# Kernel optimization log

Measured on AMD Instinct MI355X. Metric: run time of the kernel, lower is better.

The kernel has to match this reference:

```python
import jax, jax.numpy as jnp
import numpy as np

BATCH, SEQ, H, N = 8, 4096, 512, 64
DT_MIN, DT_MAX = 1e-3, 1e-1


def setup_inputs() -> dict:
    key = jax.random.key(0)
    k1, k2, k3, k4, k5 = jax.random.split(key, 5)
    n = jnp.arange(N, dtype=jnp.float32)
    # HiPPO-LegS diagonal: A[n,n] = -(n+1) -> log|diag(A)| = log(n+1)
    A_log = jnp.broadcast_to(jnp.log(n + 1.0), (H, N))
    Bv = jnp.broadcast_to(jnp.sqrt(2.0 * n + 1.0), (H, N))
    C = jax.random.normal(k1, (H, N), dtype=jnp.float32) * 0.01
    D = jnp.ones((H,), dtype=jnp.float32)
    log_dt = jax.random.uniform(k2, (H,), dtype=jnp.float32) * (
        np.log(DT_MAX) - np.log(DT_MIN)) + np.log(DT_MIN)
    # reverse-direction params (bidirectional)
    A_log_r = A_log
    B_r = Bv
    C_r = jax.random.normal(k3, (H, N), dtype=jnp.float32) * 0.01
    # out_bi Linear: weight [H, 2H], bias [H]
    W_bi = jax.random.normal(k4, (H, 2 * H), dtype=jnp.float32) / np.sqrt(2.0 * H)
    b_bi = jnp.zeros((H,), dtype=jnp.float32)
    u = jax.random.normal(k5, (BATCH, SEQ, H), dtype=jnp.float32)
    return {"u": u, "A_log": A_log, "Bv": Bv, "C": C, "D": D,
            "log_dt": log_dt, "A_log_r": A_log_r, "B_r": B_r, "C_r": C_r,
            "W_bi": W_bi, "b_bi": b_bi}


def _conv(u, A_log, Bp, Cp, D, log_dt):
    """Diagonal SSM as FFT convolution. u: [B, L, H]."""
    L = u.shape[1]
    dt = jnp.exp(log_dt)                      # [H]
    eA = jnp.exp(A_log)                       # [H, N]
    A_bar = jnp.exp(-dt[:, None] * eA)        # [H, N]
    B_bar = (A_bar - 1.0) / (-eA) * Bp        # [H, N]
    # log-space power kernel: A_bar^k = exp(k * log A_bar)
    logA = jnp.log(jnp.clip(A_bar, 1e-30, None))
    ks = jnp.arange(L, dtype=u.dtype)
    pows = jnp.exp(ks[None, None, :] * logA[:, :, None])   # [H, N, L]
    K = jnp.einsum('dn,dnl->dl', Cp * B_bar, pows)          # [H, L]
    n_fft = 2 * L
    u_f = jnp.fft.rfft(u, n=n_fft, axis=1)                  # [B, L+1, H] complex
    K_f = jnp.fft.rfft(K, n=n_fft, axis=-1)                 # [H, L+1]
    y = jnp.fft.irfft(u_f * K_f.T[None], n=n_fft, axis=1)[:, :L, :]
    return y + u * D


def reference(u, A_log, Bv, C, D, log_dt, A_log_r, B_r, C_r, W_bi, b_bi):
    y = _conv(u, A_log, Bv, C, D, log_dt)
    yr = jnp.flip(_conv(jnp.flip(u, 1), A_log_r, B_r, C_r, D, log_dt), 1)
    ycat = jnp.concatenate([y, yr], axis=-1)                # [B, L, 2H]
    return ycat @ W_bi.T + b_bi
```

## Files before the change

### kernel.cpp

```cpp
#include <hip/hip_runtime.h>
#include <hip/hip_bf16.h>
#include <stdint.h>

#define L_SEQ  4096
#define H_DIM  512
#define N_ST   64
#define N_B    8
#define N_CH   16
#define T_CH   256
#define K_GEMM 1024

typedef float  f32x4  __attribute__((ext_vector_type(4)));
typedef __bf16 bf16x8 __attribute__((ext_vector_type(8)));
typedef __bf16 bf16x4 __attribute__((ext_vector_type(4)));
typedef unsigned short u16x8 __attribute__((ext_vector_type(8)));
typedef unsigned long long ull;

#define GLOAD16(g, l) __builtin_amdgcn_global_load_lds( \
    (const __attribute__((address_space(1))) void*)(g), \
    (__attribute__((address_space(3))) void*)(l), 16, 0, 0)

__global__ __launch_bounds__(256) void k_kk(
    const float* __restrict__ A_log, const float* __restrict__ Bv,
    const float* __restrict__ C, const float* __restrict__ log_dt,
    const float* __restrict__ A_log_r, const float* __restrict__ B_r,
    const float* __restrict__ C_r,
    float* __restrict__ kk, float* __restrict__ pLG,
    float* __restrict__ pCB, float* __restrict__ pPW)
{
    __shared__ float scb[64], slg[64];
    int dirh = blockIdx.x;
    int dir  = dirh >> 9, h = dirh & 511;
    int d = threadIdx.x;
    if (d < 64) {
        int n = d;
        float dt = expf(log_dt[h]);
        const float* Al = dir ? A_log_r : A_log;
        const float* Bp = dir ? B_r    : Bv;
        const float* Cp = dir ? C_r    : C;
        float eA = expf(Al[h * N_ST + n]);
        float Ab = expf(-dt * eA);
        float Bb = (1.0f - Ab) / eA * Bp[h * N_ST + n];
        float cb = Cp[h * N_ST + n] * Bb;
        float lg = -dt * eA * 1.44269504088896f;
        scb[n] = cb; slg[n] = lg;
        pCB[dirh * 64 + n] = cb;
        pLG[dirh * 64 + n] = lg;
        pPW[dirh * 64 + n] = expf(-dt * eA * (float)T_CH);
    }
    __syncthreads();
    float s = 0.f;
    #pragma unroll
    for (int n = 0; n < 64; ++n) s += scb[n] * exp2f((float)d * slg[n]);
    kk[dirh * 256 + d] = s;
}

__global__ __launch_bounds__(256) void k_ut(
    const float* __restrict__ u, __bf16* __restrict__ ut,
    const float* __restrict__ W, __bf16* __restrict__ Wbf)
{
    __shared__ float tl[32][65];
    int blk = blockIdx.x;
    int lt = blk & 127, ht = (blk >> 7) & 7, b = blk >> 10;
    int t = threadIdx.x;
    int ho = t & 63, li = t >> 6;
    #pragma unroll
    for (int it = 0; it < 8; ++it) {
        int l = it * 4 + li;
        tl[l][ho] = u[(size_t)(b * L_SEQ + lt * 32 + l) * H_DIM + ht * 64 + ho];
    }
    if (blk < 2048) {
        int i = blk * 256 + t;
        Wbf[i] = (__bf16)W[i];
    }
    __syncthreads();
    int hh = t >> 2, lrun = (t & 3) * 8;
    bf16x8 v;
    #pragma unroll
    for (int i = 0; i < 8; ++i) v[i] = (__bf16)tl[lrun + i][hh];
    *(bf16x8*)(ut + (size_t)(ht * 64 + hh) * 32768 + b * 4096 + lt * 32 + lrun) = v;
}

__global__ __launch_bounds__(512, 2) void k_state(
    const __bf16* __restrict__ ut, const float* __restrict__ pLG,
    const float* __restrict__ pPW, __bf16* __restrict__ S2)
{
    __shared__ __bf16 uts[16384];
    int h = blockIdx.x;
    int t = threadIdx.x;
    int lane = t & 63, w = t >> 6;
    int lr = lane & 15, lg = lane >> 4;
    int dir = w >> 2, mtile = w & 3;

    float s = pLG[(size_t)(dir * 512 + h) * 64 + mtile * 16 + lr];
    f32x4 pw4 = *(const f32x4*)(pPW + (size_t)(dir * 512 + h) * 64 + mtile * 16 + lg * 4);

    bf16x8 Mf[8];
    #pragma unroll
    for (int kk = 0; kk < 8; ++kk) {
        #pragma unroll
        for (int jj = 0; jj < 8; ++jj) {
            int j = kk * 32 + lg * 8 + jj;
            float e = dir ? (float)j : (float)(255 - j);
            Mf[kk][jj] = (__bf16)exp2f(e * s);
        }
    }

    for (int hf = 0; hf < 2; ++hf) {
        if (hf) __syncthreads();
        #pragma unroll
        for (int i = 0; i < 4; ++i) {
            int chunk = i * 512 + t;
            int col   = chunk >> 5;
            int l8    = (chunk & 31) << 3;
            int l8s   = l8 ^ ((col & 7) << 3);
            GLOAD16(ut + (size_t)h * 32768 + (hf * 64 + col) * 256 + l8s,
                    (char*)uts + chunk * 16);
        }
        __syncthreads();

        #pragma unroll
        for (int ntile = 0; ntile < 4; ++ntile) {
            f32x4 acc = {};
            #pragma unroll
            for (int kk = 0; kk < 8; ++kk) {
                int col = ntile * 16 + lr;
                bf16x8 bv = *(const bf16x8*)((char*)uts + col * 512
                             + (((kk * 4 + lg) ^ (col & 7)) << 4));
                acc = __builtin_amdgcn_mfma_f32_16x16x32_bf16(Mf[kk], bv, acc, 0, 0, 0);
            }
            f32x4 X;
            if (dir == 0) {
                f32x4 incl = acc;
                float p0 = pw4[0], p1 = pw4[1], p2 = pw4[2], p3 = pw4[3];
                #pragma unroll
                for (int st = 1; st <= 8; st <<= 1) {
                    float u0 = __shfl(incl[0], (lane - st) & 63);
                    float u1 = __shfl(incl[1], (lane - st) & 63);
                    float u2 = __shfl(incl[2], (lane - st) & 63);
                    float u3 = __shfl(incl[3], (lane - st) & 63);
                    if (lr >= st) {
                        incl[0] = fmaf(p0, u0, incl[0]);
                        incl[1] = fmaf(p1, u1, incl[1]);
                        incl[2] = fmaf(p2, u2, incl[2]);
                        incl[3] = fmaf(p3, u3, incl[3]);
                    }
                    p0 *= p0; p1 *= p1; p2 *= p2; p3 *= p3;
                }
                #pragma unroll
                for (int r = 0; r < 4; ++r) {
                    float sh = __shfl(incl[r], (lane - 1) & 63);
                    X[r] = (lr == 0) ? 0.f : sh;
                }
            } else {
                f32x4 incl = acc;
                float p0 = pw4[0], p1 = pw4[1], p2 = pw4[2], p3 = pw4[3];
                #pragma unroll
                for (int st = 1; st <= 8; st <<= 1) {
                    float u0 = __shfl(incl[0], (lane + st) & 63);
                    float u1 = __shfl(incl[1], (lane + st) & 63);
                    float u2 = __shfl(incl[2], (lane + st) & 63);
                    float u3 = __shfl(incl[3], (lane + st) & 63);
                    if (lr <= 15 - st) {
                        incl[0] = fmaf(p0, u0, incl[0]);
                        incl[1] = fmaf(p1, u1, incl[1]);
                        incl[2] = fmaf(p2, u2, incl[2]);
                        incl[3] = fmaf(p3, u3, incl[3]);
                    }
                    p0 *= p0; p1 *= p1; p2 *= p2; p3 *= p3;
                }
                #pragma unroll
                for (int r = 0; r < 4; ++r) {
                    float sh = __shfl(incl[r], (lane + 1) & 63);
                    X[r] = (lr == 15) ? 0.f : sh;
                }
            }
            int colg = hf * 64 + ntile * 16 + lr;
            int nq   = mtile * 4 + lg;
            bf16x4 o;
            #pragma unroll
            for (int r = 0; r < 4; ++r) o[r] = (__bf16)X[r];
            *(bf16x4*)(S2 + ((size_t)((dir * 512 + h) * 16 + nq) * 128 + colg) * 4) = o;
        }
    }
}

template<int DIR>
__device__ __forceinline__ void conv_body(
    int h, int t,
    const float* __restrict__ kk, const float* __restrict__ pLG,
    const float* __restrict__ pCB, const float* __restrict__ Dv,
    const __bf16* __restrict__ ut, const __bf16* __restrict__ S,
    __bf16* __restrict__ ycT,
    __bf16* uts, ull* kkq8, float* slg, float* scb)
{
    int dirh = DIR * 512 + h;
    int lane = t & 63, w = t >> 6;
    int lr = lane & 15, lg = lane >> 4;

    unsigned short* asc = (unsigned short*)uts;
    for (int i = t; i < 548; i += 512) {
        int d = DIR ? (i - 272) : (271 - i);
        float kv = (d >= 0 && d < 256) ? kk[dirh * 256 + d] : 0.f;
        asc[i] = __builtin_bit_cast(unsigned short, (__bf16)kv);
    }
    if (t < 64)       slg[t]      = pLG[dirh * 64 + t];
    else if (t < 128) scb[t - 64] = pCB[dirh * 64 + (t - 64)];
    __syncthreads();
    for (int i = t; i < 544; i += 512)
        kkq8[i] = (ull)asc[i] | ((ull)asc[i+1] << 16) | ((ull)asc[i+2] << 32)
                | ((ull)asc[i+3] << 48);
    __syncthreads();

    bf16x8 gvv[2][2];
    #pragma unroll
    for (int nt = 0; nt < 2; ++nt)
        #pragma unroll
        for (int mf = 0; mf < 2; ++mf) {
            int rt = mf ? (15 - w) : w;
            int l  = rt * 16 + lr;
            float e = DIR ? (float)(256 - l) : (float)(l + 1);
            #pragma unroll
            for (int j = 0; j < 8; ++j) {
                int n = nt * 32 + lg * 8 + j;
                gvv[nt][mf][j] = (__bf16)(scb[n] * exp2f(e * slg[n]));
            }
        }

    float Dh = Dv[h];
    const ull* kq = kkq8;

    #pragma unroll
    for (int hf = 0; hf < 2; ++hf)
        #pragma unroll
        for (int i = 0; i < 4; ++i) {
            int chunk = i * 512 + t;
            int col   = chunk >> 5;
            int l8    = (chunk & 31) << 3;
            int l8s   = l8 ^ ((col & 7) << 3);
            GLOAD16(ut + (size_t)h * 32768 + (hf * 64 + col) * 256 + l8s,
                    (char*)uts + hf * 32768 + chunk * 16);
        }
    asm volatile("s_waitcnt vmcnt(4)" ::: "memory");
    __builtin_amdgcn_sched_barrier(0);
    __builtin_amdgcn_s_barrier();
    __builtin_amdgcn_sched_barrier(0);

    #pragma unroll
    for (int hf = 0; hf < 2; ++hf) {
        if (hf) __syncthreads();
        char* ub = (char*)uts + hf * 32768;

        f32x4 acc[2][4] = {};

        #pragma unroll
        for (int mf = 0; mf < 2; ++mf) {
            int rt  = mf ? (15 - w) : w;
            int jlo = DIR ? (rt >> 1) : 0;
            int jhi = DIR ? 8 : ((rt >> 1) + 1);
            int sb  = (DIR ? 272 : 271) + lg * 8 - rt * 16 - lr;
            for (int jt = jlo; jt < jhi; ++jt) {
                bf16x8 bv[4];
                #pragma unroll
                for (int n = 0; n < 4; ++n) {
                    int col = n * 16 + lr;
                    bv[n] = *(const bf16x8*)(ub + col * 512
                              + (((jt * 4 + lg) ^ (col & 7)) << 4));
                }
                int si = sb + jt * 32;
                ull lo = kq[si], hi = kq[si + 4];
                bf16x8 av;
                ((ull*)&av)[0] = lo; ((ull*)&av)[1] = hi;
                #pragma unroll
                for (int n = 0; n < 4; ++n)
                    acc[mf][n] = __builtin_amdgcn_mfma_f32_16x16x32_bf16(av, bv[n], acc[mf][n], 0, 0, 0);
            }
        }

        #pragma unroll
        for (int nt = 0; nt < 2; ++nt) {
            bf16x8 bs[4];
            #pragma unroll
            for (int n = 0; n < 4; ++n) {
                int colg = (hf * 4 + n) * 16 + lr;
                int nq0  = nt * 8 + lg * 2;
                const __bf16* sp = S + ((size_t)((DIR * 512 + h) * 16 + nq0) * 128 + colg) * 4;
                bf16x4 s0 = *(const bf16x4*)(sp);
                bf16x4 s1 = *(const bf16x4*)(sp + 512);
                #pragma unroll
                for (int j = 0; j < 4; ++j) { bs[n][j] = s0[j]; bs[n][4 + j] = s1[j]; }
            }
            #pragma unroll
            for (int mf = 0; mf < 2; ++mf)
                #pragma unroll
                for (int n = 0; n < 4; ++n)
                    acc[mf][n] = __builtin_amdgcn_mfma_f32_16x16x32_bf16(gvv[nt][mf], bs[n], acc[mf][n], 0, 0, 0);
        }

        #pragma unroll
        for (int mf = 0; mf < 2; ++mf) {
            int rt = mf ? (15 - w) : w;
            int l0 = rt * 16 + lg * 4;
            #pragma unroll
            for (int n = 0; n < 4; ++n) {
                int col = n * 16 + lr;
                bf16x4 uv = *(const bf16x4*)(ub + col * 512
                             + ((((l0 >> 3) ^ (col & 7)) << 4) | ((l0 & 7) * 2)));
                bf16x4 o;
                #pragma unroll
                for (int r = 0; r < 4; ++r)
                    o[r] = (__bf16)(acc[mf][n][r] + Dh * (float)uv[r]);
                *(bf16x4*)(ycT + (size_t)dirh * 32768 + (hf * 64 + col) * 256 + l0) = o;
            }
        }
    }
}

__global__ __launch_bounds__(512, 4) void k_conv(
    const float* __restrict__ kk, const float* __restrict__ pLG,
    const float* __restrict__ pCB, const float* __restrict__ Dv,
    const __bf16* __restrict__ ut, const __bf16* __restrict__ S,
    __bf16* __restrict__ ycT)
{
    __shared__ __bf16 uts[32768];
    __shared__ ull kkq8[544];
    __shared__ float slg[64], scb[64];
    int h = blockIdx.x & 511;
    int t = threadIdx.x;
    if (blockIdx.x >> 9)
        conv_body<1>(h, t, kk, pLG, pCB, Dv, ut, S, ycT, uts, kkq8, slg, scb);
    else
        conv_body<0>(h, t, kk, pLG, pCB, Dv, ut, S, ycT, uts, kkq8, slg, scb);
}

__global__ __launch_bounds__(256, 2) void k_gemm(
    const __bf16* __restrict__ ycT, const __bf16* __restrict__ B,
    const float* __restrict__ bias, float* __restrict__ out)
{
    __shared__ __bf16 As[2][4][128][8];
    __shared__ __bf16 Bs[2][256][32];
    int t  = threadIdx.x;
    int l  = t & 63, w = t >> 6;
    int lr = l & 15, lg = l >> 4;
    int mBase = blockIdx.y * 128;
    int nBase = blockIdx.x * 256;
    int wr = (w >> 1) * 64, wc = (w & 1) * 128;

    int sT  = t & 15;
    int sp  = t >> 4;
    int swz  = (sT & 7) << 4;
    int kgrp = sp >> 2;
    int keb  = (sp & 3) * 4;

    f32x4 acc[4][8] = {};
    const __bf16* aptr = ycT + mBase + sT * 8;

#define STAGE_A(buf, va0, va1) do { \
    char* AsB_ = (char*)&As[buf][0][0][0]; \
    _Pragma("unroll") \
    for (int i = 0; i < 8; ++i) { \
        unsigned v_ = (unsigned)(unsigned short)(va0)[i] \
                    | ((unsigned)(unsigned short)(va1)[i] << 16); \
        int off_ = ((kgrp * 128 + sT * 8 + i) * 16 + keb) ^ swz; \
        *(unsigned*)(AsB_ + off_) = v_; \
    } } while (0)

#define STAGE_B(buf, kt_) do { \
    char* BsB_ = (char*)&Bs[buf][0][0]; \
    _Pragma("unroll") \
    for (int i = 0; i < 4; ++i) { \
        int chunk_ = i * 256 + t; \
        int row_ = chunk_ >> 2, kq_ = chunk_ & 3; \
        int kqs_ = kq_ ^ ((row_ >> 1) & 3); \
        GLOAD16(B + (size_t)(nBase + row_) * K_GEMM + (kt_) + kqs_ * 8, \
                BsB_ + chunk_ * 16); \
    } } while (0)

#define COMPUTE(buf) do { \
    char* AsB_ = (char*)&As[buf][0][0][0]; \
    char* BsB_ = (char*)&Bs[buf][0][0]; \
    bf16x8 af_[4], bfv_[8]; \
    _Pragma("unroll") \
    for (int m = 0; m < 4; ++m) { \
        int row_ = wr + m * 16 + lr; \
        int off_ = ((lg * 128 + row_) * 16) ^ (((row_ >> 3) & 7) << 4); \
        af_[m] = *(const bf16x8*)(AsB_ + off_); \
    } \
    _Pragma("unroll") \
    for (int n = 0; n < 8; ++n) { \
        int row_ = wc + n * 16 + lr; \
        bfv_[n] = *(const bf16x8*)(BsB_ + row_ * 64 \
                    + ((lg * 16) ^ (((row_ >> 1) & 3) << 4))); \
    } \
    _Pragma("unroll") \
    for (int m = 0; m < 4; ++m) \
        _Pragma("unroll") \
        for (int n = 0; n < 8; ++n) \
            acc[m][n] = __builtin_amdgcn_mfma_f32_16x16x32_bf16(af_[m], bfv_[n], acc[m][n], 0, 0, 0); \
    } while (0)

    u16x8 a0 = *(const u16x8*)(aptr + (size_t)(2 * sp) * 32768);
    u16x8 a1 = *(const u16x8*)(aptr + (size_t)(2 * sp + 1) * 32768);
    STAGE_B(0, 0);

    int cur = 0;
    for (int kt = 0; kt < K_GEMM - 32; kt += 32) {
        int nxt = cur ^ 1;
        STAGE_A(cur, a0, a1);
        a0 = *(const u16x8*)(aptr + (size_t)(kt + 32 + 2 * sp) * 32768);
        a1 = *(const u16x8*)(aptr + (size_t)(kt + 32 + 2 * sp + 1) * 32768);
        STAGE_B(nxt, kt + 32);
        asm volatile("s_waitcnt vmcnt(6) lgkmcnt(0)" ::: "memory");
        __builtin_amdgcn_sched_barrier(0);
        __builtin_amdgcn_s_barrier();
        __builtin_amdgcn_sched_barrier(0);
        COMPUTE(cur);
        __builtin_amdgcn_s_barrier();
        cur ^= 1;
    }
    STAGE_A(cur, a0, a1);
    asm volatile("s_waitcnt vmcnt(0) lgkmcnt(0)" ::: "memory");
    __builtin_amdgcn_sched_barrier(0);
    __builtin_amdgcn_s_barrier();
    __builtin_amdgcn_sched_barrier(0);
    COMPUTE(cur);

#undef STAGE_A
#undef STAGE_B
#undef COMPUTE

    #pragma unroll
    for (int n = 0; n < 8; ++n) {
        int colg = nBase + wc + n * 16 + lr;
        float bv = bias[colg];
        #pragma unroll
        for (int m = 0; m < 4; ++m) {
            int rowg = mBase + wr + m * 16 + lg * 4;
            #pragma unroll
            for (int r = 0; r < 4; ++r)
                out[(size_t)(rowg + r) * H_DIM + colg] = acc[m][n][r] + bv;
        }
    }
}

extern "C" void kernel_launch(void* const* d_in, const int* in_sizes, int n_in,
                              void* d_out, int out_size, void* d_ws, size_t ws_size,
                              hipStream_t stream)
{
    const float* u       = (const float*)d_in[0];
    const float* A_log   = (const float*)d_in[1];
    const float* Bv      = (const float*)d_in[2];
    const float* C       = (const float*)d_in[3];
    const float* D       = (const float*)d_in[4];
    const float* log_dt  = (const float*)d_in[5];
    const float* A_log_r = (const float*)d_in[6];
    const float* B_r     = (const float*)d_in[7];
    const float* C_r     = (const float*)d_in[8];
    const float* W_bi    = (const float*)d_in[9];
    const float* b_bi    = (const float*)d_in[10];
    float* out = (float*)d_out;

    char* ws = (char*)d_ws;
    float* pCB  = (float*)(ws + 0x040000);
    float* pPW  = (float*)(ws + 0x080000);
    float* pLG  = (float*)(ws + 0x0C0000);
    float* kk   = (float*)(ws + 0x100000);
    __bf16* Wbf = (__bf16*)(ws + 0x200000);
    __bf16* S   = (__bf16*)(ws + 0x300000);
    __bf16* ut  = (__bf16*)(ws + 0x1300000);
    __bf16* ycT = (__bf16*)(ws + 0x3300000);

    k_kk   <<<1024, 256, 0, stream>>>(A_log, Bv, C, log_dt, A_log_r, B_r, C_r,
                                      kk, pLG, pCB, pPW);
    k_ut   <<<8192, 256, 0, stream>>>(u, ut, W_bi, Wbf);
    k_state<<<512,  512, 0, stream>>>(ut, pLG, pPW, S);
    k_conv <<<1024, 512, 0, stream>>>(kk, pLG, pCB, D, ut, S, ycT);
    dim3 g(2, 256);
    k_gemm <<<g,    256, 0, stream>>>(ycT, Wbf, b_bi, out);
}
```

Baseline: 131.0 us.

## Fuse chunk-state computation into conv kernel using shared-memory state buffer

Removes the separate k_state launch and computes per-chunk SSM states inside k_conv for each direction and half, storing them in a new shared-memory buffer instead of a global S array. This avoids a kernel launch, a second read of ut, and the global write/read round trip of the state tensor. In exchange, conv blocks do more work serially and need additional LDS and barriers, which may lower occupancy under the 4-blocks-per-CU launch bound.

```diff
diff --git a/kernel.cpp b/kernel.cpp
--- a/kernel.cpp
+++ b/kernel.cpp
@@ -81,33 +81,67 @@
     *(bf16x8*)(ut + (size_t)(ht * 64 + hh) * 32768 + b * 4096 + lt * 32 + lrun) = v;
 }
 
-__global__ __launch_bounds__(512, 2) void k_state(
-    const __bf16* __restrict__ ut, const float* __restrict__ pLG,
-    const float* __restrict__ pPW, __bf16* __restrict__ S2)
-{
-    __shared__ __bf16 uts[16384];
-    int h = blockIdx.x;
-    int t = threadIdx.x;
+template<int DIR>
+__device__ __forceinline__ void conv_body(
+    int h, int t,
+    const float* __restrict__ kk, const float* __restrict__ pLG,
+    const float* __restrict__ pCB, const float* __restrict__ pPW,
+    const float* __restrict__ Dv,
+    const __bf16* __restrict__ ut, __bf16* __restrict__ ycT,
+    __bf16* uts, ull* kkq8, __bf16* Sx, float* slg, float* scb)
+{
+    int dirh = DIR * 512 + h;
     int lane = t & 63, w = t >> 6;
     int lr = lane & 15, lg = lane >> 4;
-    int dir = w >> 2, mtile = w & 3;
-
-    float s = pLG[(size_t)(dir * 512 + h) * 64 + mtile * 16 + lr];
-    f32x4 pw4 = *(const f32x4*)(pPW + (size_t)(dir * 512 + h) * 64 + mtile * 16 + lg * 4);
-
+
+    unsigned short* asc = (unsigned short*)uts;
+    for (int i = t; i < 548; i += 512) {
+        int d = DIR ? (i - 272) : (271 - i);
+        float kv = (d >= 0 && d < 256) ? kk[dirh * 256 + d] : 0.f;
+        asc[i] = __builtin_bit_cast(unsigned short, (__bf16)kv);
+    }
+    if (t < 64)       slg[t]      = pLG[dirh * 64 + t];
+    else if (t < 128) scb[t - 64] = pCB[dirh * 64 + (t - 64)];
+    __syncthreads();
+    for (int i = t; i < 544; i += 512)
+        kkq8[i] = (ull)asc[i] | ((ull)asc[i+1] << 16) | ((ull)asc[i+2] << 32)
+                | ((ull)asc[i+3] << 48);
+    __syncthreads();
+
+    bf16x8 gvv[2][2];
+    #pragma unroll
+    for (int nt = 0; nt < 2; ++nt)
+        #pragma unroll
+        for (int mf = 0; mf < 2; ++mf) {
+            int rt = mf ? (15 - w) : w;
+            int l  = rt * 16 + lr;
+            float e = DIR ? (float)(256 - l) : (float)(l + 1);
+            #pragma unroll
+            for (int j = 0; j < 8; ++j) {
+                int n = nt * 32 + lg * 8 + j;
+                gvv[nt][mf][j] = (__bf16)(scb[n] * exp2f(e * slg[n]));
+            }
+        }
+
+    int mtile = w >> 1;
+    float sm = slg[mtile * 16 + lr];
+    f32x4 pw4 = *(const f32x4*)(pPW + (size_t)dirh * 64 + mtile * 16 + lg * 4);
     bf16x8 Mf[8];
     #pragma unroll
-    for (int kk = 0; kk < 8; ++kk) {
+    for (int kq_ = 0; kq_ < 8; ++kq_) {
         #pragma unroll
         for (int jj = 0; jj < 8; ++jj) {
-            int j = kk * 32 + lg * 8 + jj;
-            float e = dir ? (float)j : (float)(255 - j);
-            Mf[kk][jj] = (__bf16)exp2f(e * s);
-        }
-    }
-
-    for (int hf = 0; hf < 2; ++hf) {
-        if (hf) __syncthreads();
+            int j = kq_ * 32 + lg * 8 + jj;
+            float e = DIR ? (float)j : (float)(255 - j);
+            Mf[kq_][jj] = (__bf16)exp2f(e * sm);
+        }
+    }
+
+    float Dh = Dv[h];
+    const ull* kq = kkq8;
+
+    #pragma unroll
+    for (int hf = 0; hf < 2; ++hf)
         #pragma unroll
         for (int i = 0; i < 4; ++i) {
             int chunk = i * 512 + t;
@@ -115,22 +149,31 @@
             int l8    = (chunk & 31) << 3;
             int l8s   = l8 ^ ((col & 7) << 3);
             GLOAD16(ut + (size_t)h * 32768 + (hf * 64 + col) * 256 + l8s,
-                    (char*)uts + chunk * 16);
-        }
-        __syncthreads();
-
-        #pragma unroll
-        for (int ntile = 0; ntile < 4; ++ntile) {
+                    (char*)uts + hf * 32768 + chunk * 16);
+        }
+    asm volatile("s_waitcnt vmcnt(4)" ::: "memory");
+    __builtin_amdgcn_sched_barrier(0);
+    __builtin_amdgcn_s_barrier();
+    __builtin_amdgcn_sched_barrier(0);
+
+    #pragma unroll
+    for (int hf = 0; hf < 2; ++hf) {
+        if (hf) __syncthreads();
+        char* ub = (char*)uts + hf * 32768;
+
+        #pragma unroll
+        for (int qq = 0; qq < 2; ++qq) {
+            int ntile = (w & 1) * 2 + qq;
             f32x4 acc = {};
             #pragma unroll
-            for (int kk = 0; kk < 8; ++kk) {
+            for (int kk_ = 0; kk_ < 8; ++kk_) {
                 int col = ntile * 16 + lr;
-                bf16x8 bv = *(const bf16x8*)((char*)uts + col * 512
-                             + (((kk * 4 + lg) ^ (col & 7)) << 4));
-                acc = __builtin_amdgcn_mfma_f32_16x16x32_bf16(Mf[kk], bv, acc, 0, 0, 0);
+                bf16x8 bv = *(const bf16x8*)(ub + col * 512
+                             + (((kk_ * 4 + lg) ^ (col & 7)) << 4));
+                acc = __builtin_amdgcn_mfma_f32_16x16x32_bf16(Mf[kk_], bv, acc, 0, 0, 0);
             }
             f32x4 X;
-            if (dir == 0) {
+            if (DIR == 0) {
                 f32x4 incl = acc;
                 float p0 = pw4[0], p1 = pw4[1], p2 = pw4[2], p3 = pw4[3];
                 #pragma unroll
@@ -175,81 +218,14 @@
                     X[r] = (lr == 15) ? 0.f : sh;
                 }
             }
-            int colg = hf * 64 + ntile * 16 + lr;
+            int colx = ntile * 16 + lr;
             int nq   = mtile * 4 + lg;
             bf16x4 o;
             #pragma unroll
             for (int r = 0; r < 4; ++r) o[r] = (__bf16)X[r];
-            *(bf16x4*)(S2 + ((size_t)((dir * 512 + h) * 16 + nq) * 128 + colg) * 4) = o;
-        }
-    }
-}
-
-template<int DIR>
-__device__ __forceinline__ void conv_body(
-    int h, int t,
-    const float* __restrict__ kk, const float* __restrict__ pLG,
-    const float* __restrict__ pCB, const float* __restrict__ Dv,
-    const __bf16* __restrict__ ut, const __bf16* __restrict__ S,
-    __bf16* __restrict__ ycT,
-    __bf16* uts, ull* kkq8, float* slg, float* scb)
-{
-    int dirh = DIR * 512 + h;
-    int lane = t & 63, w = t >> 6;
-    int lr = lane & 15, lg = lane >> 4;
-
-    unsigned short* asc = (unsigned short*)uts;
-    for (int i = t; i < 548; i += 512) {
-        int d = DIR ? (i - 272) : (271 - i);
-        float kv = (d >= 0 && d < 256) ? kk[dirh * 256 + d] : 0.f;
-        asc[i] = __builtin_bit_cast(unsigned short, (__bf16)kv);
-    }
-    if (t < 64)       slg[t]      = pLG[dirh * 64 + t];
-    else if (t < 128) scb[t - 64] = pCB[dirh * 64 + (t - 64)];
-    __syncthreads();
-    for (int i = t; i < 544; i += 512)
-        kkq8[i] = (ull)asc[i] | ((ull)asc[i+1] << 16) | ((ull)asc[i+2] << 32)
-                | ((ull)asc[i+3] << 48);
-    __syncthreads();
-
-    bf16x8 gvv[2][2];
-    #pragma unroll
-    for (int nt = 0; nt < 2; ++nt)
-        #pragma unroll
-        for (int mf = 0; mf < 2; ++mf) {
-            int rt = mf ? (15 - w) : w;
-            int l  = rt * 16 + lr;
-            float e = DIR ? (float)(256 - l) : (float)(l + 1);
-            #pragma unroll
-            for (int j = 0; j < 8; ++j) {
-                int n = nt * 32 + lg * 8 + j;
-                gvv[nt][mf][j] = (__bf16)(scb[n] * exp2f(e * slg[n]));
-            }
-        }
-
-    float Dh = Dv[h];
-    const ull* kq = kkq8;
-
-    #pragma unroll
-    for (int hf = 0; hf < 2; ++hf)
-        #pragma unroll
-        for (int i = 0; i < 4; ++i) {
-            int chunk = i * 512 + t;
-            int col   = chunk >> 5;
-            int l8    = (chunk & 31) << 3;
-            int l8s   = l8 ^ ((col & 7) << 3);
-            GLOAD16(ut + (size_t)h * 32768 + (hf * 64 + col) * 256 + l8s,
-                    (char*)uts + hf * 32768 + chunk * 16);
-        }
-    asm volatile("s_waitcnt vmcnt(4)" ::: "memory");
-    __builtin_amdgcn_sched_barrier(0);
-    __builtin_amdgcn_s_barrier();
-    __builtin_amdgcn_sched_barrier(0);
-
-    #pragma unroll
-    for (int hf = 0; hf < 2; ++hf) {
-        if (hf) __syncthreads();
-        char* ub = (char*)uts + hf * 32768;
+            *(bf16x4*)(Sx + ((size_t)nq * 64 + colx) * 4) = o;
+        }
+        __syncthreads();
 
         f32x4 acc[2][4] = {};
 
@@ -282,11 +258,11 @@
             bf16x8 bs[4];
             #pragma unroll
             for (int n = 0; n < 4; ++n) {
-                int colg = (hf * 4 + n) * 16 + lr;
+                int colx = n * 16 + lr;
                 int nq0  = nt * 8 + lg * 2;
-                const __bf16* sp = S + ((size_t)((DIR * 512 + h) * 16 + nq0) * 128 + colg) * 4;
+                const __bf16* sp = Sx + ((size_t)nq0 * 64 + colx) * 4;
                 bf16x4 s0 = *(const bf16x4*)(sp);
-                bf16x4 s1 = *(const bf16x4*)(sp + 512);
+                bf16x4 s1 = *(const bf16x4*)(sp + 256);
                 #pragma unroll
                 for (int j = 0; j < 4; ++j) { bs[n][j] = s0[j]; bs[n][4 + j] = s1[j]; }
             }
@@ -318,19 +294,20 @@
 
 __global__ __launch_bounds__(512, 4) void k_conv(
     const float* __restrict__ kk, const float* __restrict__ pLG,
-    const float* __restrict__ pCB, const float* __restrict__ Dv,
-    const __bf16* __restrict__ ut, const __bf16* __restrict__ S,
-    __bf16* __restrict__ ycT)
+    const float* __restrict__ pCB, const float* __restrict__ pPW,
+    const float* __restrict__ Dv,
+    const __bf16* __restrict__ ut, __bf16* __restrict__ ycT)
 {
     __shared__ __bf16 uts[32768];
     __shared__ ull kkq8[544];
+    __shared__ __bf16 Sx[4096];
     __shared__ float slg[64], scb[64];
     int h = blockIdx.x & 511;
     int t = threadIdx.x;
     if (blockIdx.x >> 9)
-        conv_body<1>(h, t, kk, pLG, pCB, Dv, ut, S, ycT, uts, kkq8, slg, scb);
+        conv_body<1>(h, t, kk, pLG, pCB, pPW, Dv, ut, ycT, uts, kkq8, Sx, slg, scb);
     else
-        conv_body<0>(h, t, kk, pLG, pCB, Dv, ut, S, ycT, uts, kkq8, slg, scb);
+        conv_body<0>(h, t, kk, pLG, pCB, pPW, Dv, ut, ycT, uts, kkq8, Sx, slg, scb);
 }
 
 __global__ __launch_bounds__(256, 2) void k_gemm(
@@ -466,15 +443,13 @@
     float* pLG  = (float*)(ws + 0x0C0000);
     float* kk   = (float*)(ws + 0x100000);
     __bf16* Wbf = (__bf16*)(ws + 0x200000);
-    __bf16* S   = (__bf16*)(ws + 0x300000);
     __bf16* ut  = (__bf16*)(ws + 0x1300000);
     __bf16* ycT = (__bf16*)(ws + 0x3300000);
 
     k_kk   <<<1024, 256, 0, stream>>>(A_log, Bv, C, log_dt, A_log_r, B_r, C_r,
                                       kk, pLG, pCB, pPW);
     k_ut   <<<8192, 256, 0, stream>>>(u, ut, W_bi, Wbf);
-    k_state<<<512,  512, 0, stream>>>(ut, pLG, pPW, S);
-    k_conv <<<1024, 512, 0, stream>>>(kk, pLG, pCB, D, ut, S, ycT);
+    k_conv <<<1024, 512, 0, stream>>>(kk, pLG, pCB, pPW, D, ut, ycT);
     dim3 g(2, 256);
     k_gemm <<<g,    256, 0, stream>>>(ycT, Wbf, b_bi, out);
 }
```

Result: slower. 142.5 us (+8.8%).

## Merge kernel-precompute into transpose launch and triple-buffer GEMM B tiles

Applied to the files above, without the earlier changes.

Folds the SSM kernel/parameter precompute into the u-transpose launch as extra blocks, removing one kernel launch and letting the two independent jobs share the GPU. The GEMM now keeps three B-tile LDS buffers with a prefetch distance of two k-steps (vmcnt relaxed accordingly), and remaps block IDs so neighbouring blocks land on different M rows, aiming at better L2/channel locality. Uses more LDS per GEMM block, which may affect occupancy at two blocks per CU, and the epilogue is hand-unrolled.

```diff
diff --git a/kernel.cpp b/kernel.cpp
--- a/kernel.cpp
+++ b/kernel.cpp
@@ -20,7 +20,9 @@
     (const __attribute__((address_space(1))) void*)(g), \
     (__attribute__((address_space(3))) void*)(l), 16, 0, 0)
 
-__global__ __launch_bounds__(256) void k_kk(
+__global__ __launch_bounds__(256) void k_ut(
+    const float* __restrict__ u, __bf16* __restrict__ ut,
+    const float* __restrict__ W, __bf16* __restrict__ Wbf,
     const float* __restrict__ A_log, const float* __restrict__ Bv,
     const float* __restrict__ C, const float* __restrict__ log_dt,
     const float* __restrict__ A_log_r, const float* __restrict__ B_r,
@@ -28,41 +30,40 @@
     float* __restrict__ kk, float* __restrict__ pLG,
     float* __restrict__ pCB, float* __restrict__ pPW)
 {
+    __shared__ float tl[32][65];
     __shared__ float scb[64], slg[64];
-    int dirh = blockIdx.x;
-    int dir  = dirh >> 9, h = dirh & 511;
-    int d = threadIdx.x;
-    if (d < 64) {
-        int n = d;
-        float dt = expf(log_dt[h]);
-        const float* Al = dir ? A_log_r : A_log;
-        const float* Bp = dir ? B_r    : Bv;
-        const float* Cp = dir ? C_r    : C;
-        float eA = expf(Al[h * N_ST + n]);
-        float Ab = expf(-dt * eA);
-        float Bb = (1.0f - Ab) / eA * Bp[h * N_ST + n];
-        float cb = Cp[h * N_ST + n] * Bb;
-        float lg = -dt * eA * 1.44269504088896f;
-        scb[n] = cb; slg[n] = lg;
-        pCB[dirh * 64 + n] = cb;
-        pLG[dirh * 64 + n] = lg;
-        pPW[dirh * 64 + n] = expf(-dt * eA * (float)T_CH);
-    }
-    __syncthreads();
-    float s = 0.f;
-    #pragma unroll
-    for (int n = 0; n < 64; ++n) s += scb[n] * exp2f((float)d * slg[n]);
-    kk[dirh * 256 + d] = s;
-}
-
-__global__ __launch_bounds__(256) void k_ut(
-    const float* __restrict__ u, __bf16* __restrict__ ut,
-    const float* __restrict__ W, __bf16* __restrict__ Wbf)
-{
-    __shared__ float tl[32][65];
     int blk = blockIdx.x;
+    int t = threadIdx.x;
+
+    if (blk >= 8192) {
+        int dirh = blk - 8192;
+        int dir  = dirh >> 9, h = dirh & 511;
+        int d = t;
+        if (d < 64) {
+            int n = d;
+            float dt = expf(log_dt[h]);
+            const float* Al = dir ? A_log_r : A_log;
+            const float* Bp = dir ? B_r    : Bv;
+            const float* Cp = dir ? C_r    : C;
+            float eA = expf(Al[h * N_ST + n]);
+            float Ab = expf(-dt * eA);
+            float Bb = (1.0f - Ab) / eA * Bp[h * N_ST + n];
+            float cb = Cp[h * N_ST + n] * Bb;
+            float lg = -dt * eA * 1.44269504088896f;
+            scb[n] = cb; slg[n] = lg;
+            pCB[dirh * 64 + n] = cb;
+            pLG[dirh * 64 + n] = lg;
+            pPW[dirh * 64 + n] = expf(-dt * eA * (float)T_CH);
+        }
+        __syncthreads();
+        float s = 0.f;
+        #pragma unroll
+        for (int n = 0; n < 64; ++n) s += scb[n] * exp2f((float)d * slg[n]);
+        kk[dirh * 256 + d] = s;
+        return;
+    }
+
     int lt = blk & 127, ht = (blk >> 7) & 7, b = blk >> 10;
-    int t = threadIdx.x;
     int ho = t & 63, li = t >> 6;
     #pragma unroll
     for (int it = 0; it < 8; ++it) {
@@ -338,12 +339,14 @@
     const float* __restrict__ bias, float* __restrict__ out)
 {
     __shared__ __bf16 As[2][4][128][8];
-    __shared__ __bf16 Bs[2][256][32];
+    __shared__ __bf16 Bs[3][256][32];
     int t  = threadIdx.x;
     int l  = t & 63, w = t >> 6;
     int lr = l & 15, lg = l >> 4;
-    int mBase = blockIdx.y * 128;
-    int nBase = blockIdx.x * 256;
+    int bid   = blockIdx.y * 2 + blockIdx.x;
+    int swzid = (bid & 7) * 64 + (bid >> 3);
+    int mBase = (swzid >> 1) * 128;
+    int nBase = (swzid & 1) * 256;
     int wr = (w >> 1) * 64, wc = (w & 1) * 128;
 
     int sT  = t & 15;
@@ -355,8 +358,8 @@
     f32x4 acc[4][8] = {};
     const __bf16* aptr = ycT + mBase + sT * 8;
 
-#define STAGE_A(buf, va0, va1) do { \
-    char* AsB_ = (char*)&As[buf][0][0][0]; \
+#define STAGE_A(abuf, va0, va1) do { \
+    char* AsB_ = (char*)&As[0][0][0][0] + (abuf) * 8192; \
     _Pragma("unroll") \
     for (int i = 0; i < 8; ++i) { \
         unsigned v_ = (unsigned)(unsigned short)(va0)[i] \
@@ -365,8 +368,8 @@
         *(unsigned*)(AsB_ + off_) = v_; \
     } } while (0)
 
-#define STAGE_B(buf, kt_) do { \
-    char* BsB_ = (char*)&Bs[buf][0][0]; \
+#define STAGE_B(bbuf, kt_) do { \
+    char* BsB_ = (char*)&Bs[0][0][0] + (bbuf) * 16384; \
     _Pragma("unroll") \
     for (int i = 0; i < 4; ++i) { \
         int chunk_ = i * 256 + t; \
@@ -376,9 +379,9 @@
                 BsB_ + chunk_ * 16); \
     } } while (0)
 
-#define COMPUTE(buf) do { \
-    char* AsB_ = (char*)&As[buf][0][0][0]; \
-    char* BsB_ = (char*)&Bs[buf][0][0]; \
+#define COMPUTE(abuf, bbuf) do { \
+    char* AsB_ = (char*)&As[0][0][0][0] + (abuf) * 8192; \
+    char* BsB_ = (char*)&Bs[0][0][0] + (bbuf) * 16384; \
     bf16x8 af_[4], bfv_[8]; \
     _Pragma("unroll") \
     for (int m = 0; m < 4; ++m) { \
@@ -402,28 +405,41 @@
     u16x8 a0 = *(const u16x8*)(aptr + (size_t)(2 * sp) * 32768);
     u16x8 a1 = *(const u16x8*)(aptr + (size_t)(2 * sp + 1) * 32768);
     STAGE_B(0, 0);
-
-    int cur = 0;
-    for (int kt = 0; kt < K_GEMM - 32; kt += 32) {
-        int nxt = cur ^ 1;
-        STAGE_A(cur, a0, a1);
+    STAGE_B(1, 32);
+
+    int ab = 0, cb = 0, sb = 2;
+    for (int kt = 0; kt <= 928; kt += 32) {
+        STAGE_A(ab, a0, a1);
         a0 = *(const u16x8*)(aptr + (size_t)(kt + 32 + 2 * sp) * 32768);
         a1 = *(const u16x8*)(aptr + (size_t)(kt + 32 + 2 * sp + 1) * 32768);
-        STAGE_B(nxt, kt + 32);
-        asm volatile("s_waitcnt vmcnt(6) lgkmcnt(0)" ::: "memory");
+        STAGE_B(sb, kt + 64);
+        asm volatile("s_waitcnt vmcnt(10) lgkmcnt(0)" ::: "memory");
         __builtin_amdgcn_sched_barrier(0);
         __builtin_amdgcn_s_barrier();
         __builtin_amdgcn_sched_barrier(0);
-        COMPUTE(cur);
+        COMPUTE(ab, cb);
         __builtin_amdgcn_s_barrier();
-        cur ^= 1;
-    }
-    STAGE_A(cur, a0, a1);
+        ab ^= 1;
+        cb = (cb == 2) ? 0 : cb + 1;
+        sb = (sb == 2) ? 0 : sb + 1;
+    }
+    STAGE_A(ab, a0, a1);
+    a0 = *(const u16x8*)(aptr + (size_t)(992 + 2 * sp) * 32768);
+    a1 = *(const u16x8*)(aptr + (size_t)(992 + 2 * sp + 1) * 32768);
+    asm volatile("s_waitcnt vmcnt(6) lgkmcnt(0)" ::: "memory");
+    __builtin_amdgcn_sched_barrier(0);
+    __builtin_amdgcn_s_barrier();
+    __builtin_amdgcn_sched_barrier(0);
+    COMPUTE(ab, cb);
+    __builtin_amdgcn_s_barrier();
+    ab ^= 1;
+    cb = (cb == 2) ? 0 : cb + 1;
+    STAGE_A(ab, a0, a1);
     asm volatile("s_waitcnt vmcnt(0) lgkmcnt(0)" ::: "memory");
     __builtin_amdgcn_sched_barrier(0);
     __builtin_amdgcn_s_barrier();
     __builtin_amdgcn_sched_barrier(0);
-    COMPUTE(cur);
+    COMPUTE(ab, cb);
 
 #undef STAGE_A
 #undef STAGE_B
@@ -470,9 +486,9 @@
     __bf16* ut  = (__bf16*)(ws + 0x1300000);
     __bf16* ycT = (__bf16*)(ws + 0x3300000);
 
-    k_kk   <<<1024, 256, 0, stream>>>(A_log, Bv, C, log_dt, A_log_r, B_r, C_r,
+    k_ut   <<<9216, 256, 0, stream>>>(u, ut, W_bi, Wbf,
+                                      A_log, Bv, C, log_dt, A_log_r, B_r, C_r,
                                       kk, pLG, pCB, pPW);
-    k_ut   <<<8192, 256, 0, stream>>>(u, ut, W_bi, Wbf);
     k_state<<<512,  512, 0, stream>>>(ut, pLG, pPW, S);
     k_conv <<<1024, 512, 0, stream>>>(kk, pLG, pCB, D, ut, S, ycT);
     dim3 g(2, 256);
```

Result: no change. 128.5 us (-1.9%).
